# Kernel optimization log

Hardware: AMD Instinct MI355X
Metric: run time of the kernel (lower is better)

Reference implementation:

```python
import jax, jax.numpy as jnp
import numpy as np
from jax import lax

B, T, N, F, K = 8, 16, 1024, 128, 4


def setup_inputs() -> dict:
    key = jax.random.key(0)
    k1, k2, k3, k4 = jax.random.split(key, 4)
    x = jax.random.normal(k1, (B, T, N, F), dtype=jnp.float32)
    # shift operator scaled so its spectral radius is ~1 (stable powers L^1..L^K)
    L = jax.random.normal(k2, (N, N), dtype=jnp.float32) / jnp.sqrt(jnp.float32(N))
    # xavier_uniform with relu gain: limit = gain * sqrt(6/(fan_in+fan_out))
    gain = jnp.sqrt(jnp.float32(2.0))
    lim = gain * jnp.sqrt(6.0 / (F + F))
    W = jax.random.uniform(k3, (K, F, F), dtype=jnp.float32, minval=-lim, maxval=lim)
    H = jax.random.uniform(k4, (K, F, F), dtype=jnp.float32, minval=-lim, maxval=lim)
    return {"x": x, "L": L, "W": W, "H": H}


def reference(x, L, W, H):
    """Recurrent graph-polynomial filter.

    h_t = relu( sum_{k=0}^{K-1} L^{k+1} @ (x_t @ W[k] + h_{t-1} @ H[k]) ), h_{-1}=0.
    Matches the torch loop where alpha_k starts at L and is multiplied by L each tap.
    """
    Kt = W.shape[0]
    # powers L^1 .. L^K, stacked [K, N, N]
    pows = [L]
    for _ in range(1, Kt):
        pows.append(pows[-1] @ L)
    Lp = jnp.stack(pows)

    def step(h, x_t):
        # x_t, h: [B, N, F]
        s = jnp.einsum('bnf,kfg->kbng', x_t, W) + jnp.einsum('bnf,kfg->kbng', h, H)
        z = jnp.einsum('knm,kbmg->bng', Lp, s)
        h_new = jax.nn.relu(z)
        return h_new, h_new

    xT = jnp.swapaxes(x, 0, 1)          # [T, B, N, F]
    h0 = jnp.zeros_like(x[:, 0])        # [B, N, F]
    _, outs = lax.scan(step, h0, xT)    # [T, B, N, F]
    return jnp.swapaxes(outs, 0, 1)     # [B, T, N, F]
```

## Files before the change

kernel.cpp:

```cpp
#include <hip/hip_runtime.h>
#include <stdint.h>


typedef __bf16 bf16_t;
typedef __bf16 bf16x4 __attribute__((ext_vector_type(4)));
typedef __bf16 bf16x8 __attribute__((ext_vector_type(8)));
typedef float  f32x4  __attribute__((ext_vector_type(4)));
typedef float  f32x16 __attribute__((ext_vector_type(16)));

__device__ __forceinline__ void gload_lds16(const void* g, void* l) {
    __builtin_amdgcn_global_load_lds(
        (const __attribute__((address_space(1))) void*)g,
        (__attribute__((address_space(3))) void*)l,
        16, 0, 0);
}


__global__ void k_convert_x(const float* __restrict__ xin,
                            bf16_t* __restrict__ xb, int n4) {
    int i = blockIdx.x * 256 + threadIdx.x;
    int stride = gridDim.x * 256;
    for (; i < n4; i += stride) {
        float4 v = reinterpret_cast<const float4*>(xin)[i];
        bf16x4 o = { (bf16_t)v.x, (bf16_t)v.y, (bf16_t)v.z, (bf16_t)v.w };
        reinterpret_cast<bf16x4*>(xb)[i] = o;
    }
}

__global__ void k_setup_L(const float* __restrict__ L,
                          bf16_t* __restrict__ Lcat,
                          bf16_t* __restrict__ Lt) {
    int idx = blockIdx.x * 256 + threadIdx.x;
    int n = idx >> 10, m = idx & 1023;
    float v = L[idx];
    Lcat[n * 4096 + m] = (bf16_t)v;
    Lt[m * 1024 + n]   = (bf16_t)v;
}

__global__ void k_setup_WH(const float* __restrict__ W,
                           const float* __restrict__ H,
                           bf16_t* __restrict__ WHT) {
    int idx = blockIdx.x * 256 + threadIdx.x;
    int k = idx >> 14, f = (idx >> 7) & 127, g = idx & 127;
    WHT[(k * 128 + g) * 256 + f]       = (bf16_t)W[idx];
    WHT[(k * 128 + g) * 256 + 128 + f] = (bf16_t)H[idx];
}


template<int NZ>
__global__ __launch_bounds__(256)
void k_combine(const float* __restrict__ Zp,
               bf16_t* __restrict__ h, float* __restrict__ out, int t) {
    int i = blockIdx.x * 256 + threadIdx.x;
    int n  = i >> 8;
    int cg = (i & 255) * 4;
    size_t o = (size_t)n * 1024 + cg;
    float4 s = *reinterpret_cast<const float4*>(Zp + o);
    #pragma unroll
    for (int z = 1; z < NZ; ++z) {
        float4 v = *reinterpret_cast<const float4*>(Zp + (size_t)z * 1048576 + o);
        s.x += v.x; s.y += v.y; s.z += v.z; s.w += v.w;
    }
    s.x = fmaxf(s.x, 0.f); s.y = fmaxf(s.y, 0.f);
    s.z = fmaxf(s.z, 0.f); s.w = fmaxf(s.w, 0.f);
    int b = cg >> 7, g = cg & 127;
    size_t ho = (size_t)b * 131072 + (size_t)n * 128 + g;
    bf16x4 hb = { (bf16_t)s.x, (bf16_t)s.y, (bf16_t)s.z, (bf16_t)s.w };
    *reinterpret_cast<bf16x4*>(h + ho) = hb;
    *reinterpret_cast<float4*>(out + (size_t)b * 2097152
                                   + (size_t)t * 131072
                                   + (size_t)n * 128 + g) = s;
}

template<int BM, int BN, int GX, int GY, int GZ, int KTOT,
         int EPI, int BADDR, int ZK, int DEC>
__global__ __launch_bounds__(256)
void k_gemm(const bf16_t* __restrict__ A, int lda,
            const bf16_t* __restrict__ BT, int ldbt,
            const bf16_t* __restrict__ B2,
            bf16_t* __restrict__ Cb, float* __restrict__ Cf,
            int ldc, int t)
{
    constexpr int BK = 64;
    constexpr int WM = BM / 2, WN = BN / 2;
    constexpr int MF = WM / 32, NF = WN / 32;
    constexpr int NT = KTOT / BK;
    constexpr int NWG = GX * GY * GZ;
    constexpr int ACH = BM * 8;
    constexpr int BCH = BN * 8;

    __shared__ __align__(16) bf16_t As[2][BM * BK];
    __shared__ __align__(16) bf16_t Bs[2][BN * BK];

    const int tid  = threadIdx.x;
    const int lane = tid & 63;
    const int wave = tid >> 6;
    const int wm = wave >> 1, wn = wave & 1;

    const int id  = blockIdx.x;
    const int swz = (id & 7) * (NWG / 8) + (id >> 3);
    int bx, by, bz;
    if (DEC == 0) {
        bx = swz % GX; by = (swz / GX) % GY; bz = swz / (GX * GY);
    } else {
        by = swz % GY; bz = (swz / GY) % GZ; bx = swz / (GY * GZ);
    }

    const int m0 = by * BM;
    const int c0 = bx * BN;
    const int kb_ = bz;

    const bf16_t* Ap = (EPI == 1) ? (A + kb_ * 128 * 256) : A;

    f32x16 acc[MF][NF] = {};

    auto stage = [&](int bufi, int kt) {
        const int q0 = kt * BK + (ZK > 0 ? kb_ * ZK : 0);
        #pragma unroll
        for (int i = 0; i < ACH / 256; ++i) {
            int chunk = i * 256 + tid;
            int off = chunk * 16;
            int row = off >> 7;
            int kel = ((off ^ ((row & 7) << 4)) & 127) >> 1;
            const bf16_t* src = Ap + (size_t)(m0 + row) * lda + (q0 + kel);
            gload_lds16(src, (char*)(&As[bufi][0]) + off);
        }
        #pragma unroll
        for (int i = 0; i < BCH / 256; ++i) {
            int chunk = i * 256 + tid;
            int off = chunk * 16;
            int row = off >> 7;
            int kel = ((off ^ ((row & 7) << 4)) & 127) >> 1;
            int c = c0 + row;
            const bf16_t* src;
            if (BADDR == 0) {
                src = BT + (size_t)c * ldbt + (q0 + kel);
            } else {
                int f = q0 + kel;
                if (q0 < 128) {
                    src = BT + (size_t)(c >> 10) * 2097152
                             + (size_t)t * 131072
                             + (size_t)(c & 1023) * 128 + f;
                } else {
                    src = B2 + (size_t)c * 128 + (f - 128);
                }
            }
            gload_lds16(src, (char*)(&Bs[bufi][0]) + off);
        }
    };

    stage(0, 0);
    asm volatile("s_waitcnt vmcnt(0)" ::: "memory");
    __syncthreads();

    for (int kt = 0; kt < NT; ++kt) {
        int cur = kt & 1;
        if (kt + 1 < NT) stage(cur ^ 1, kt + 1);

        #pragma unroll
        for (int kk = 0; kk < 4; ++kk) {
            bf16x8 af[MF], bfr[NF];
            const int klane = kk * 32 + (lane >> 5) * 16;
            #pragma unroll
            for (int mf = 0; mf < MF; ++mf) {
                int row = wm * WM + mf * 32 + (lane & 31);
                int bo = (row * 128 + klane) ^ ((row & 7) << 4);
                af[mf] = *reinterpret_cast<const bf16x8*>(
                             (const char*)(&As[cur][0]) + bo);
            }
            #pragma unroll
            for (int nf = 0; nf < NF; ++nf) {
                int row = wn * WN + nf * 32 + (lane & 31);
                int bo = (row * 128 + klane) ^ ((row & 7) << 4);
                bfr[nf] = *reinterpret_cast<const bf16x8*>(
                              (const char*)(&Bs[cur][0]) + bo);
            }
            #pragma unroll
            for (int mf = 0; mf < MF; ++mf)
                #pragma unroll
                for (int nf = 0; nf < NF; ++nf)
                    acc[mf][nf] = __builtin_amdgcn_mfma_f32_32x32x16_bf16(
                        af[mf], bfr[nf], acc[mf][nf], 0, 0, 0);
        }

        asm volatile("s_waitcnt vmcnt(0)" ::: "memory");
        __syncthreads();
    }

    #pragma unroll
    for (int mf = 0; mf < MF; ++mf) {
        #pragma unroll
        for (int nf = 0; nf < NF; ++nf) {
            f32x16 v = acc[mf][nf];
            int col   = c0 + wn * WN + nf * 32 + (lane & 31);
            int rbase = m0 + wm * WM + mf * 32 + 4 * (lane >> 5);
            #pragma unroll
            for (int r = 0; r < 16; ++r) {
                int row = rbase + (r & 3) + 8 * (r >> 2);
                float val = v[r];
                if (EPI == 0) {
                    Cb[(size_t)row * ldc + col] = (bf16_t)val;
                } else if (EPI == 1) {
                    Cb[(size_t)(col >> 10) * 524288 + (size_t)row * 4096
                       + (size_t)kb_ * 1024 + (col & 1023)] = (bf16_t)val;
                } else if (EPI == 2) {
                    val = fmaxf(val, 0.f);
                    int b = col >> 7, g = col & 127;
                    Cb[(size_t)b * 131072 + (size_t)row * 128 + g] = (bf16_t)val;
                    Cf[(size_t)b * 2097152 + (size_t)t * 131072
                       + (size_t)row * 128 + g] = val;
                } else {
                    Cf[(size_t)kb_ * 1048576 + (size_t)row * 1024 + col] = val;
                }
            }
        }
    }
}


extern "C" void kernel_launch(void* const* d_in, const int* in_sizes, int n_in,
                              void* d_out, int out_size, void* d_ws, size_t ws_size,
                              hipStream_t stream) {
    const float* x = (const float*)d_in[0];
    const float* L = (const float*)d_in[1];
    const float* W = (const float*)d_in[2];
    const float* H = (const float*)d_in[3];
    float* out = (float*)d_out;

    char* ws = (char*)d_ws;
    bf16_t* xb   = (bf16_t*)(ws);
    bf16_t* Lcat = (bf16_t*)(ws + 33554432);
    bf16_t* Lt   = (bf16_t*)(ws + 41943040);
    bf16_t* WHT  = (bf16_t*)(ws + 44040192);
    bf16_t* Sbuf = (bf16_t*)(ws + 44302336);
    bf16_t* h    = (bf16_t*)(ws + 52690944);
    float*  Zp   = (float*) (ws + 54788096);
    if (ws_size < 54788096u) return;
    const bool bigws = (ws_size >= 88342528u);

    hipMemsetAsync(h, 0, 2097152, stream);
    k_convert_x<<<4096, 256, 0, stream>>>(x, xb, 16777216 / 4);
    k_setup_L <<<4096, 256, 0, stream>>>(L, Lcat, Lt);
    k_setup_WH<<<256, 256, 0, stream>>>(W, H, WHT);

    for (int p = 1; p < 4; ++p) {
        k_gemm<64, 64, 16, 16, 1, 1024, 0, 0, 0, 0><<<256, 256, 0, stream>>>(
            Lcat + (p - 1) * 1024, 4096, Lt, 1024, nullptr,
            Lcat + p * 1024, nullptr, 4096, 0);
    }

    for (int t = 0; t < 16; ++t) {
        k_gemm<64, 128, 64, 2, 4, 256, 1, 1, 0, 1><<<512, 256, 0, stream>>>(
            WHT, 256, xb, 0, h,
            Sbuf, nullptr, 0, t);
        if (bigws) {
            k_gemm<128, 128, 8, 8, 8, 512, 3, 0, 512, 0><<<512, 256, 0, stream>>>(
                Lcat, 4096, Sbuf, 4096, nullptr,
                nullptr, Zp, 0, t);
            k_combine<8><<<1024, 256, 0, stream>>>(Zp, h, out, t);
        } else {
            k_gemm<128, 128, 8, 8, 1, 4096, 2, 0, 0, 0><<<64, 256, 0, stream>>>(
                Lcat, 4096, Sbuf, 4096, nullptr,
                h, out, 0, t);
        }
    }
}
```

Measured before the change: 558.9 us.

## Triple-buffer GEMM pipeline and rebalance graph GEMM split-K to four slices

Moves the GEMM main loop from double to triple buffering in LDS, using partial vmcnt waits so two tiles are in flight and only one barrier is taken per iteration. It also changes the graph GEMM to 128x64 tiles with a 4-way split-K, so the combine kernel now reduces 4 partials instead of 8. The goal is to hide global-load latency and cut Zp partial traffic and reduction work. In exchange it uses more LDS, which may lower occupancy, and the hard-coded vmcnt counts depend on loads per thread.

```diff
diff --git a/kernel.cpp b/kernel.cpp
--- a/kernel.cpp
+++ b/kernel.cpp
@@ -47,7 +47,6 @@
 }
 
 
-template<int NZ>
 __global__ __launch_bounds__(256)
 void k_combine(const float* __restrict__ Zp,
                bf16_t* __restrict__ h, float* __restrict__ out, int t) {
@@ -55,14 +54,15 @@
     int n  = i >> 8;
     int cg = (i & 255) * 4;
     size_t o = (size_t)n * 1024 + cg;
-    float4 s = *reinterpret_cast<const float4*>(Zp + o);
-    #pragma unroll
-    for (int z = 1; z < NZ; ++z) {
-        float4 v = *reinterpret_cast<const float4*>(Zp + (size_t)z * 1048576 + o);
-        s.x += v.x; s.y += v.y; s.z += v.z; s.w += v.w;
-    }
-    s.x = fmaxf(s.x, 0.f); s.y = fmaxf(s.y, 0.f);
-    s.z = fmaxf(s.z, 0.f); s.w = fmaxf(s.w, 0.f);
+    float4 v0 = *reinterpret_cast<const float4*>(Zp + o);
+    float4 v1 = *reinterpret_cast<const float4*>(Zp + 1048576 + o);
+    float4 v2 = *reinterpret_cast<const float4*>(Zp + 2097152 + o);
+    float4 v3 = *reinterpret_cast<const float4*>(Zp + 3145728 + o);
+    float4 s;
+    s.x = fmaxf(v0.x + v1.x + v2.x + v3.x, 0.f);
+    s.y = fmaxf(v0.y + v1.y + v2.y + v3.y, 0.f);
+    s.z = fmaxf(v0.z + v1.z + v2.z + v3.z, 0.f);
+    s.w = fmaxf(v0.w + v1.w + v2.w + v3.w, 0.f);
     int b = cg >> 7, g = cg & 127;
     size_t ho = (size_t)b * 131072 + (size_t)n * 128 + g;
     bf16x4 hb = { (bf16_t)s.x, (bf16_t)s.y, (bf16_t)s.z, (bf16_t)s.w };
@@ -74,12 +74,12 @@
 
 template<int BM, int BN, int GX, int GY, int GZ, int KTOT,
          int EPI, int BADDR, int ZK, int DEC>
-__global__ __launch_bounds__(256)
-void k_gemm(const bf16_t* __restrict__ A, int lda,
-            const bf16_t* __restrict__ BT, int ldbt,
-            const bf16_t* __restrict__ B2,
-            bf16_t* __restrict__ Cb, float* __restrict__ Cf,
-            int ldc, int t)
+__device__ __forceinline__
+void gemm_body(const bf16_t* __restrict__ A, int lda,
+               const bf16_t* __restrict__ BT, int ldbt,
+               const bf16_t* __restrict__ B2,
+               bf16_t* __restrict__ Cb, float* __restrict__ Cf,
+               int ldc, int t)
 {
     constexpr int BK = 64;
     constexpr int WM = BM / 2, WN = BN / 2;
@@ -88,9 +88,10 @@
     constexpr int NWG = GX * GY * GZ;
     constexpr int ACH = BM * 8;
     constexpr int BCH = BN * 8;
-
-    __shared__ __align__(16) bf16_t As[2][BM * BK];
-    __shared__ __align__(16) bf16_t Bs[2][BN * BK];
+    constexpr int LPT = (ACH + BCH) / 256;
+
+    __shared__ __align__(16) bf16_t As[3][BM * BK];
+    __shared__ __align__(16) bf16_t Bs[3][BN * BK];
 
     const int tid  = threadIdx.x;
     const int lane = tid & 63;
@@ -150,13 +151,25 @@
     };
 
     stage(0, 0);
-    asm volatile("s_waitcnt vmcnt(0)" ::: "memory");
-    __syncthreads();
+    stage(1, 1);
 
     for (int kt = 0; kt < NT; ++kt) {
-        int cur = kt & 1;
-        if (kt + 1 < NT) stage(cur ^ 1, kt + 1);
-
+        if (kt < NT - 1) {
+            if constexpr (LPT == 4)
+                asm volatile("s_waitcnt vmcnt(4)" ::: "memory");
+            else if constexpr (LPT == 6)
+                asm volatile("s_waitcnt vmcnt(6)" ::: "memory");
+            else
+                asm volatile("s_waitcnt vmcnt(8)" ::: "memory");
+        } else {
+            asm volatile("s_waitcnt vmcnt(0)" ::: "memory");
+        }
+        __builtin_amdgcn_s_barrier();
+        __builtin_amdgcn_sched_barrier(0);
+
+        if (kt + 2 < NT) stage((kt + 2) % 3, kt + 2);
+
+        const int cur = kt % 3;
         #pragma unroll
         for (int kk = 0; kk < 4; ++kk) {
             bf16x8 af[MF], bfr[NF];
@@ -182,9 +195,7 @@
                     acc[mf][nf] = __builtin_amdgcn_mfma_f32_32x32x16_bf16(
                         af[mf], bfr[nf], acc[mf][nf], 0, 0, 0);
         }
-
-        asm volatile("s_waitcnt vmcnt(0)" ::: "memory");
-        __syncthreads();
+        __builtin_amdgcn_sched_barrier(0);
     }
 
     #pragma unroll
@@ -218,6 +229,35 @@
 }
 
 
+__global__ __launch_bounds__(256)
+void k_chain(const bf16_t* __restrict__ A, const bf16_t* __restrict__ BT,
+             bf16_t* __restrict__ Cb) {
+    gemm_body<64, 64, 16, 16, 1, 1024, 0, 0, 0, 0>(
+        A, 4096, BT, 1024, nullptr, Cb, nullptr, 4096, 0);
+}
+
+__global__ __launch_bounds__(256)
+void k_feat(const bf16_t* __restrict__ WHT, const bf16_t* __restrict__ xb,
+            const bf16_t* __restrict__ h, bf16_t* __restrict__ Sbuf, int t) {
+    gemm_body<64, 128, 64, 2, 4, 256, 1, 1, 0, 1>(
+        WHT, 256, xb, 0, h, Sbuf, nullptr, 0, t);
+}
+
+__global__ __launch_bounds__(256)
+void k_graph(const bf16_t* __restrict__ Lcat, const bf16_t* __restrict__ Sbuf,
+             float* __restrict__ Zp) {
+    gemm_body<128, 64, 16, 8, 4, 1024, 3, 0, 1024, 0>(
+        Lcat, 4096, Sbuf, 4096, nullptr, nullptr, Zp, 0, 0);
+}
+
+__global__ __launch_bounds__(256)
+void k_graph_ns(const bf16_t* __restrict__ Lcat, const bf16_t* __restrict__ Sbuf,
+                bf16_t* __restrict__ h, float* __restrict__ out, int t) {
+    gemm_body<128, 128, 8, 8, 1, 4096, 2, 0, 0, 0>(
+        Lcat, 4096, Sbuf, 4096, nullptr, h, out, 0, t);
+}
+
+
 extern "C" void kernel_launch(void* const* d_in, const int* in_sizes, int n_in,
                               void* d_out, int out_size, void* d_ws, size_t ws_size,
                               hipStream_t stream) {
@@ -236,7 +276,7 @@
     bf16_t* h    = (bf16_t*)(ws + 52690944);
     float*  Zp   = (float*) (ws + 54788096);
     if (ws_size < 54788096u) return;
-    const bool bigws = (ws_size >= 88342528u);
+    const bool bigws = (ws_size >= 71565312u);
 
     hipMemsetAsync(h, 0, 2097152, stream);
     k_convert_x<<<4096, 256, 0, stream>>>(x, xb, 16777216 / 4);
@@ -244,24 +284,17 @@
     k_setup_WH<<<256, 256, 0, stream>>>(W, H, WHT);
 
     for (int p = 1; p < 4; ++p) {
-        k_gemm<64, 64, 16, 16, 1, 1024, 0, 0, 0, 0><<<256, 256, 0, stream>>>(
-            Lcat + (p - 1) * 1024, 4096, Lt, 1024, nullptr,
-            Lcat + p * 1024, nullptr, 4096, 0);
+        k_chain<<<256, 256, 0, stream>>>(Lcat + (p - 1) * 1024, Lt,
+                                         Lcat + p * 1024);
     }
 
     for (int t = 0; t < 16; ++t) {
-        k_gemm<64, 128, 64, 2, 4, 256, 1, 1, 0, 1><<<512, 256, 0, stream>>>(
-            WHT, 256, xb, 0, h,
-            Sbuf, nullptr, 0, t);
+        k_feat<<<512, 256, 0, stream>>>(WHT, xb, h, Sbuf, t);
         if (bigws) {
-            k_gemm<128, 128, 8, 8, 8, 512, 3, 0, 512, 0><<<512, 256, 0, stream>>>(
-                Lcat, 4096, Sbuf, 4096, nullptr,
-                nullptr, Zp, 0, t);
-            k_combine<8><<<1024, 256, 0, stream>>>(Zp, h, out, t);
+            k_graph<<<512, 256, 0, stream>>>(Lcat, Sbuf, Zp);
+            k_combine<<<1024, 256, 0, stream>>>(Zp, h, out, t);
         } else {
-            k_gemm<128, 128, 8, 8, 1, 4096, 2, 0, 0, 0><<<64, 256, 0, stream>>>(
-                Lcat, 4096, Sbuf, 4096, nullptr,
-                h, out, 0, t);
-        }
-    }
-}
+            k_graph_ns<<<64, 256, 0, stream>>>(Lcat, Sbuf, h, out, t);
+        }
+    }
+}
```

Result: faster. 519.4 us (-7.1%).
